# Optimization experiments

Hardware: AMD Instinct MI355X
Metric: run time of the kernel (lower is better)

The kernel has to match this reference:

```python
import jax, jax.numpy as jnp
import numpy as np

N_USERS = 100000
N_ITEMS = 50000
N_NODES = N_USERS + N_ITEMS
N_EDGES = 2400000
EMB = 64
LEAKY_ALPHA = 0.3  # tf.keras.layers.LeakyReLU default


def setup_inputs() -> dict:
    key = jax.random.key(0)
    ks = jax.random.split(key, 7)
    return {
        "user_emb": jax.random.normal(ks[0], (N_USERS, EMB), dtype=jnp.float32) * 0.1,
        "item_emb": jax.random.normal(ks[1], (N_ITEMS, EMB), dtype=jnp.float32) * 0.1,
        "W0": jax.random.normal(ks[2], (EMB, EMB), dtype=jnp.float32) * (1.0 / np.sqrt(EMB)),
        "W1": jax.random.normal(ks[3], (EMB, EMB), dtype=jnp.float32) * (1.0 / np.sqrt(EMB)),
        "adj_vals": jax.random.uniform(ks[4], (N_EDGES,), dtype=jnp.float32),
        "adj_rows": jax.random.randint(ks[5], (N_EDGES,), 0, N_NODES, dtype=jnp.int32),
        "adj_cols": jax.random.randint(ks[6], (N_EDGES,), 0, N_NODES, dtype=jnp.int32),
    }


def reference(user_emb, item_emb, W0, W1, adj_vals, adj_rows, adj_cols):
    n_users = user_emb.shape[0]
    n_nodes = n_users + item_emb.shape[0]

    def spmm(e):  # sparse adjacency @ dense embeddings, COO form
        # gather source-node features, scale by edge weight, scatter-add to dest rows
        return jax.ops.segment_sum(adj_vals[:, None] * e[adj_cols], adj_rows,
                                   num_segments=n_nodes)

    e0 = jnp.concatenate([user_emb, item_emb], axis=0)          # [N, d]
    # gcn[0] = GraphConv(W0): transpose(W0 @ (A@e)^T) == (A@e) @ W0^T
    e1 = spmm(e0) @ W0.T
    # gcn[1] = LeakyReLU (Keras default alpha=0.3)
    e2 = jnp.where(e1 >= 0, e1, LEAKY_ALPHA * e1)
    # gcn[2] = GraphConv(W1)
    e3 = spmm(e2) @ W1.T
    # stack+mean over the 4 embedding stages
    all_emb = (e0 + e1 + e2 + e3) * 0.25
    return all_emb[:n_users], all_emb[n_users:]
```

## Files before the change

kernel.cpp:

```cpp
#include <hip/hip_runtime.h>

#define N_USERS 100000
#define N_ITEMS 50000
#define N_NODES 150000
#define N_EDGES 2400000
#define EMB 64
#define LEAKY 0.3f

#define RB_SHIFT 8
#define RB (1 << RB_SHIFT)
#define NBKT ((N_NODES + RB - 1) >> RB_SHIFT)
#define L1_CHUNK 16384
#define NCH ((N_EDGES + L1_CHUNK - 1) / L1_CHUNK)
#define COL_MASK 0x3FFFFu
#define NTILE (N_NODES / 16)

typedef unsigned short u16;
typedef unsigned int   u32;
typedef __attribute__((ext_vector_type(8))) short short8v;
typedef __attribute__((ext_vector_type(4))) float f32x4;
typedef __attribute__((ext_vector_type(2))) float v2f;

__device__ __forceinline__ u16 f32_to_bf16_rne(float f) {
    u32 u = __float_as_uint(f);
    u32 r = (u + 0x7FFFu + ((u >> 16) & 1u)) >> 16;
    return (u16)r;
}
__device__ __forceinline__ float bf16_lo(u32 x) { return __uint_as_float(x << 16); }
__device__ __forceinline__ u32 pack_bf16(float lo, float hi) {
    return (u32)f32_to_bf16_rne(lo) | ((u32)f32_to_bf16_rne(hi) << 16);
}
__device__ __forceinline__ v2f up2(u32 w) {
    v2f r;
    r.x = __uint_as_float(w << 16);
    r.y = __uint_as_float(w & 0xFFFF0000u);
    return r;
}

__global__ __launch_bounds__(256) void conv_all(
    const float* __restrict__ uemb, const float* __restrict__ iemb,
    const float* __restrict__ W0, const float* __restrict__ W1,
    u16* __restrict__ ebf, u16* __restrict__ Wbf0, u16* __restrict__ Wbf1)
{
    const int gid = blockIdx.x * 256 + threadIdx.x;
    const int i = gid * 4;
    if (i < N_NODES * EMB) {
        const float* src = (i < N_USERS * EMB) ? uemb + i : iemb + (i - N_USERS * EMB);
        const float4 v = *(const float4*)src;
        ushort4 w;
        w.x = f32_to_bf16_rne(v.x);
        w.y = f32_to_bf16_rne(v.y);
        w.z = f32_to_bf16_rne(v.z);
        w.w = f32_to_bf16_rne(v.w);
        *(ushort4*)(ebf + i) = w;
    }
    if (gid < EMB * EMB) {
        Wbf0[gid] = f32_to_bf16_rne(W0[gid]);
        Wbf1[gid] = f32_to_bf16_rne(W1[gid]);
    }
}

__global__ __launch_bounds__(1024) void bkt_hist(
    const int* __restrict__ rows, int* __restrict__ H)
{
    __shared__ int cnt[NBKT];
    const int t = threadIdx.x;
    const int c = blockIdx.x;
    if (t < NBKT) cnt[t] = 0;
    __syncthreads();

    const int e0 = c * L1_CHUNK;
    const int e1 = (e0 + L1_CHUNK < N_EDGES) ? e0 + L1_CHUNK : N_EDGES;
    for (int i = e0 + t; i < e1; i += 1024)
        atomicAdd(&cnt[rows[i] >> RB_SHIFT], 1);
    __syncthreads();

    if (t < NBKT) H[c * NBKT + t] = cnt[t];
}

__global__ __launch_bounds__(1024) void scan_bkt(
    const int* __restrict__ H, int* __restrict__ bkt_ptr)
{
    __shared__ int lds[1024];
    const int t = threadIdx.x;

    int tot = 0;
    if (t < NBKT) {
        int a0 = 0, a1 = 0, a2 = 0, a3 = 0;
        int c = 0;
        for (; c + 4 <= NCH; c += 4) {
            a0 += H[(c + 0) * NBKT + t];
            a1 += H[(c + 1) * NBKT + t];
            a2 += H[(c + 2) * NBKT + t];
            a3 += H[(c + 3) * NBKT + t];
        }
        for (; c < NCH; ++c) a0 += H[c * NBKT + t];
        tot = (a0 + a1) + (a2 + a3);
    }
    lds[t] = (t < NBKT) ? tot : 0;
    __syncthreads();
    for (int off = 1; off < 1024; off <<= 1) {
        int x = 0;
        if (t >= off) x = lds[t - off];
        __syncthreads();
        lds[t] += x;
        __syncthreads();
    }
    if (t < NBKT) bkt_ptr[t] = lds[t] - tot;
    if (t == 0) bkt_ptr[NBKT] = N_EDGES;
}

__global__ __launch_bounds__(256) void fill_B(
    const int* __restrict__ H, const int* __restrict__ bkt_ptr,
    int* __restrict__ B)
{
    const int b = blockIdx.x * 256 + threadIdx.x;
    if (b >= NBKT) return;
    int run = bkt_ptr[b];
    int c = 0;
    for (; c + 4 <= NCH; c += 4) {
        const int h0 = H[(c + 0) * NBKT + b];
        const int h1 = H[(c + 1) * NBKT + b];
        const int h2 = H[(c + 2) * NBKT + b];
        const int h3 = H[(c + 3) * NBKT + b];
        B[(c + 0) * NBKT + b] = run;
        B[(c + 1) * NBKT + b] = run + h0;
        B[(c + 2) * NBKT + b] = run + h0 + h1;
        B[(c + 3) * NBKT + b] = run + h0 + h1 + h2;
        run += h0 + h1 + h2 + h3;
    }
    for (; c < NCH; ++c) {
        B[c * NBKT + b] = run;
        run += H[c * NBKT + b];
    }
}

__global__ __launch_bounds__(1024) void partition_l1(
    const float* __restrict__ vals, const int* __restrict__ rows,
    const int* __restrict__ cols, const int* __restrict__ B,
    float2* __restrict__ svc)
{
    __shared__ int base[NBKT];
    __shared__ int cnt[NBKT];
    const int t = threadIdx.x;
    const int c = blockIdx.x;
    if (t < NBKT) {
        base[t] = B[c * NBKT + t];
        cnt[t]  = 0;
    }
    __syncthreads();

    const int e0 = c * L1_CHUNK;
    const int e1 = (e0 + L1_CHUNK < N_EDGES) ? e0 + L1_CHUNK : N_EDGES;
    for (int i = e0 + t; i < e1; i += 1024) {
        const int r = rows[i];
        const int b = r >> RB_SHIFT;
        const int pos = base[b] + atomicAdd(&cnt[b], 1);
        const u32 packed = ((u32)(r & (RB - 1)) << 18) | (u32)cols[i];
        svc[pos] = make_float2(vals[i], __uint_as_float(packed));
    }
}

__global__ __launch_bounds__(512) void place_l2(
    const int* __restrict__ bkt_ptr, const float2* __restrict__ svc,
    float2* __restrict__ sedge, int* __restrict__ row_ptr)
{
    __shared__ int cnt[RB];
    __shared__ int heads[RB];
    const int b     = blockIdx.x;
    const int rbase = b << RB_SHIFT;
    const int t     = threadIdx.x;

    if (t < RB) cnt[t] = 0;
    __syncthreads();

    const int lo = bkt_ptr[b];
    const int hi = bkt_ptr[b + 1];

    for (int i = lo + t; i < hi; i += 512)
        atomicAdd(&cnt[__float_as_uint(svc[i].y) >> 18], 1);
    __syncthreads();

    int v = 0;
    if (t < RB) v = cnt[t];
    for (int off = 1; off < RB; off <<= 1) {
        int x = 0;
        if (t < RB && t >= off) x = cnt[t - off];
        __syncthreads();
        if (t < RB) cnt[t] += x;
        __syncthreads();
    }
    if (t < RB) {
        const int excl = cnt[t] - v;
        heads[t] = lo + excl;
        const int gr = rbase + t;
        if (gr <= N_NODES) row_ptr[gr] = lo + excl;
    }
    __syncthreads();

    for (int i = lo + t; i < hi; i += 512) {
        const float2 vc = svc[i];
        const int lr  = (int)(__float_as_uint(vc.y) >> 18);
        const int pos = atomicAdd(&heads[lr], 1);
        sedge[pos] = vc;
    }
}

__global__ __launch_bounds__(256) void spmm_bf16(
    const int* __restrict__ row_ptr,
    const float2* __restrict__ sedge,
    const u16* __restrict__ ebf,
    u16* __restrict__ tbf)
{
    const int tid  = threadIdx.x;
    const int lane = tid & 63;
    const int row  = blockIdx.x * 4 + (tid >> 6);
    if (row >= N_NODES) return;

    const int g = lane >> 3;
    const int q = lane & 7;

    const int beg = row_ptr[row];
    const int end = row_ptr[row + 1];

    v2f A0 = {0.f, 0.f}, A1 = {0.f, 0.f}, A2 = {0.f, 0.f}, A3 = {0.f, 0.f};

    for (int k = beg; k < end; k += 16) {
        const int  kA  = k + g;
        const int  kB  = k + 8 + g;
        const bool onA = kA < end;
        const bool onB = kB < end;
        const float2 mA = sedge[onA ? kA : end - 1];
        const float2 mB = sedge[onB ? kB : end - 1];
        const float vA = onA ? mA.x : 0.f;
        const float vB = onB ? mB.x : 0.f;
        const u32 iA = __float_as_uint(mA.y) & COL_MASK;
        const u32 iB = __float_as_uint(mB.y) & COL_MASK;
        const uint4 xA = *((const uint4*)(ebf + (size_t)iA * EMB) + q);
        const uint4 xB = *((const uint4*)(ebf + (size_t)iB * EMB) + q);
        const v2f vvA = {vA, vA};
        const v2f vvB = {vB, vB};
        A0 = vvA * up2(xA.x) + A0;
        A1 = vvA * up2(xA.y) + A1;
        A2 = vvA * up2(xA.z) + A2;
        A3 = vvA * up2(xA.w) + A3;
        A0 = vvB * up2(xB.x) + A0;
        A1 = vvB * up2(xB.y) + A1;
        A2 = vvB * up2(xB.z) + A2;
        A3 = vvB * up2(xB.w) + A3;
    }

    float s0 = A0.x, s1 = A0.y, s2 = A1.x, s3 = A1.y;
    float s4 = A2.x, s5 = A2.y, s6 = A3.x, s7 = A3.y;
    s0 += __shfl_xor(s0, 8); s0 += __shfl_xor(s0, 16); s0 += __shfl_xor(s0, 32);
    s1 += __shfl_xor(s1, 8); s1 += __shfl_xor(s1, 16); s1 += __shfl_xor(s1, 32);
    s2 += __shfl_xor(s2, 8); s2 += __shfl_xor(s2, 16); s2 += __shfl_xor(s2, 32);
    s3 += __shfl_xor(s3, 8); s3 += __shfl_xor(s3, 16); s3 += __shfl_xor(s3, 32);
    s4 += __shfl_xor(s4, 8); s4 += __shfl_xor(s4, 16); s4 += __shfl_xor(s4, 32);
    s5 += __shfl_xor(s5, 8); s5 += __shfl_xor(s5, 16); s5 += __shfl_xor(s5, 32);
    s6 += __shfl_xor(s6, 8); s6 += __shfl_xor(s6, 16); s6 += __shfl_xor(s6, 32);
    s7 += __shfl_xor(s7, 8); s7 += __shfl_xor(s7, 16); s7 += __shfl_xor(s7, 32);

    if (g == 0) {
        uint4 w;
        w.x = pack_bf16(s0, s1);
        w.y = pack_bf16(s2, s3);
        w.z = pack_bf16(s4, s5);
        w.w = pack_bf16(s6, s7);
        *(uint4*)(tbf + (size_t)row * EMB + 8 * q) = w;
    }
}

template <bool FIRST>
__global__ __launch_bounds__(256) void dense_mfma(
    const u16* __restrict__ tbf,
    const u16* __restrict__ Wbf,
    u16* ebf,
    u16* __restrict__ obf,
    float* __restrict__ out)
{
    const int tid  = threadIdx.x;
    const int l    = tid & 63;
    const int tile = blockIdx.x * 4 + (tid >> 6);
    if (tile >= NTILE) return;
    const int row0 = tile * 16;

    const int lr = l & 15;
    const int lk = l >> 4;

    short8v bfrag[4][2];
    #pragma unroll
    for (int c = 0; c < 4; ++c)
        #pragma unroll
        for (int kh = 0; kh < 2; ++kh)
            bfrag[c][kh] = *(const short8v*)(Wbf + (size_t)(16 * c + lr) * EMB
                                             + 32 * kh + 8 * lk);

    const u16* trow = tbf + (size_t)(row0 + lr) * EMB;
    const short8v afrag0 = *(const short8v*)(trow + 8 * lk);
    const short8v afrag1 = *(const short8v*)(trow + 32 + 8 * lk);

    f32x4 acc[4];
    #pragma unroll
    for (int c = 0; c < 4; ++c) {
        f32x4 z = {0.f, 0.f, 0.f, 0.f};
        z = __builtin_amdgcn_mfma_f32_16x16x32_bf16(afrag0, bfrag[c][0], z, 0, 0, 0);
        z = __builtin_amdgcn_mfma_f32_16x16x32_bf16(afrag1, bfrag[c][1], z, 0, 0, 0);
        acc[c] = z;
    }

    #pragma unroll
    for (int c = 0; c < 4; ++c) {
        #pragma unroll
        for (int r = 0; r < 4; ++r) {
            const int row = row0 + 4 * lk + r;
            const size_t idx = (size_t)row * EMB + 16 * c + lr;
            const float e1v = acc[c][r];
            if (FIRST) {
                const float e2v = (e1v >= 0.f) ? e1v : LEAKY * e1v;
                const float e0v = bf16_lo((u32)ebf[idx]);
                obf[idx] = f32_to_bf16_rne(0.25f * (e0v + e1v + e2v));
                ebf[idx] = f32_to_bf16_rne(e2v);
            } else {
                out[idx] = bf16_lo((u32)obf[idx]) + 0.25f * e1v;
            }
        }
    }
}

__global__ __launch_bounds__(256) void spmm_atomic(
    const float* __restrict__ vals, const int* __restrict__ rows,
    const int* __restrict__ cols, const float* __restrict__ src_a,
    const float* __restrict__ src_b, float* __restrict__ dst)
{
    const int tid  = threadIdx.x;
    const int lane = tid & 63;
    const int e    = blockIdx.x * 4 + (tid >> 6);
    if (e >= N_EDGES) return;
    const float v = vals[e];
    const int   c = cols[e];
    const int   r = rows[e];
    const float* src = (src_b != nullptr && c >= N_USERS)
                           ? src_b + (size_t)(c - N_USERS) * EMB
                           : src_a + (size_t)c * EMB;
    unsafeAtomicAdd(&dst[(size_t)r * EMB + lane], v * src[lane]);
}

template <bool FIRST>
__global__ __launch_bounds__(256) void dense_f32(
    const float* __restrict__ t, const float* __restrict__ W,
    const float* __restrict__ user_emb, const float* __restrict__ item_emb,
    float* __restrict__ e2, float* __restrict__ out)
{
    __shared__ float wT[64][65];
    __shared__ float trow[16][64];

    const int tid = threadIdx.x;
    for (int k = tid; k < 64 * 64; k += 256) {
        const int i = k >> 6, j = k & 63;
        wT[j][i] = W[k];
    }
    const int row_base = blockIdx.x * 16;
    for (int k = tid; k < 16 * 64; k += 256) {
        const int r = k >> 6, j = k & 63;
        const int row = row_base + r;
        trow[r][j] = (row < N_NODES) ? t[(size_t)row * EMB + j] : 0.f;
    }
    __syncthreads();

    const int i  = tid & 63;
    const int r0 = tid >> 6;

    #pragma unroll
    for (int rr = 0; rr < 4; ++rr) {
        const int r   = r0 * 4 + rr;
        const int row = row_base + r;
        if (row >= N_NODES) continue;
        float acc = 0.f;
        #pragma unroll
        for (int j = 0; j < 64; ++j)
            acc = fmaf(trow[r][j], wT[j][i], acc);
        const size_t idx = (size_t)row * EMB + i;
        if (FIRST) {
            const float e1v = acc;
            const float e2v = (e1v >= 0.f) ? e1v : LEAKY * e1v;
            const float e0v = (row < N_USERS)
                                  ? user_emb[idx]
                                  : item_emb[(size_t)(row - N_USERS) * EMB + i];
            e2[idx]  = e2v;
            out[idx] = 0.25f * (e0v + e1v + e2v);
        } else {
            out[idx] += 0.25f * acc;
        }
    }
}

extern "C" void kernel_launch(void* const* d_in, const int* in_sizes, int n_in,
                              void* d_out, int out_size, void* d_ws, size_t ws_size,
                              hipStream_t stream)
{
    const float* user_emb = (const float*)d_in[0];
    const float* item_emb = (const float*)d_in[1];
    const float* W0       = (const float*)d_in[2];
    const float* W1       = (const float*)d_in[3];
    const float* adj_vals = (const float*)d_in[4];
    const int*   adj_rows = (const int*)d_in[5];
    const int*   adj_cols = (const int*)d_in[6];
    float*       out      = (float*)d_out;

    const size_t mat_bytes = (size_t)N_NODES * EMB * sizeof(float);
    const size_t ebf_bytes = (size_t)N_NODES * EMB * sizeof(u16);
    const size_t edge8     = (size_t)N_EDGES * sizeof(float2);
    const size_t hmat      = (size_t)NCH * NBKT * sizeof(int);

    const size_t off_tbf    = 0;
    const size_t off_svc    = 0;
    const size_t off_sedge  = off_tbf + ebf_bytes;
    const size_t off_ebf    = off_sedge + edge8;
    const size_t off_obf    = off_ebf + ebf_bytes;
    const size_t off_rowptr = off_obf + ebf_bytes;
    const size_t off_H      = off_rowptr + (size_t)(N_NODES + 1) * sizeof(int);
    const size_t off_B      = off_H + hmat;
    const size_t off_ptr    = off_B + hmat;
    const size_t off_wbf    = (off_ptr + (size_t)(NBKT + 1) * sizeof(int) + 15) & ~(size_t)15;
    const size_t required   = off_wbf + 2 * (size_t)EMB * EMB * sizeof(u16);

    const int spmm_blocks   = (N_NODES + 3) / 4;
    const int densem_blocks = (NTILE + 3) / 4;
    const int conv_blocks   = (N_NODES * EMB / 4 + 255) / 256;

    if (ws_size >= required) {
        u16*    tbf     = (u16*)((char*)d_ws + off_tbf);
        float2* svc     = (float2*)((char*)d_ws + off_svc);
        float2* sedge   = (float2*)((char*)d_ws + off_sedge);
        u16*    ebf     = (u16*)((char*)d_ws + off_ebf);
        u16*    obf     = (u16*)((char*)d_ws + off_obf);
        int*    row_ptr = (int*)((char*)d_ws + off_rowptr);
        int*    H       = (int*)((char*)d_ws + off_H);
        int*    B       = (int*)((char*)d_ws + off_B);
        int*    bkt_ptr = (int*)((char*)d_ws + off_ptr);
        u16*    Wbf0    = (u16*)((char*)d_ws + off_wbf);
        u16*    Wbf1    = Wbf0 + EMB * EMB;

        conv_all<<<conv_blocks, 256, 0, stream>>>(
            user_emb, item_emb, W0, W1, ebf, Wbf0, Wbf1);

        bkt_hist<<<NCH, 1024, 0, stream>>>(adj_rows, H);
        scan_bkt<<<1, 1024, 0, stream>>>(H, bkt_ptr);
        fill_B<<<(NBKT + 255) / 256, 256, 0, stream>>>(H, bkt_ptr, B);
        partition_l1<<<NCH, 1024, 0, stream>>>(
            adj_vals, adj_rows, adj_cols, B, svc);
        place_l2<<<NBKT, 512, 0, stream>>>(bkt_ptr, svc, sedge, row_ptr);

        spmm_bf16<<<spmm_blocks, 256, 0, stream>>>(row_ptr, sedge, ebf, tbf);
        dense_mfma<true><<<densem_blocks, 256, 0, stream>>>(
            tbf, Wbf0, ebf, obf, out);

        spmm_bf16<<<spmm_blocks, 256, 0, stream>>>(row_ptr, sedge, ebf, tbf);
        dense_mfma<false><<<densem_blocks, 256, 0, stream>>>(
            tbf, Wbf1, ebf, obf, out);
    } else {
        float* t  = (float*)d_ws;
        float* e2 = (float*)((char*)d_ws + mat_bytes);
        const int dense_blocks = (N_NODES + 15) / 16;

        hipMemsetAsync(t, 0, mat_bytes, stream);
        spmm_atomic<<<(N_EDGES + 3) / 4, 256, 0, stream>>>(
            adj_vals, adj_rows, adj_cols, user_emb, item_emb, t);
        dense_f32<true><<<dense_blocks, 256, 0, stream>>>(
            t, W0, user_emb, item_emb, e2, out);

        hipMemsetAsync(t, 0, mat_bytes, stream);
        spmm_atomic<<<(N_EDGES + 3) / 4, 256, 0, stream>>>(
            adj_vals, adj_rows, adj_cols, e2, nullptr, t);
        dense_f32<false><<<dense_blocks, 256, 0, stream>>>(
            t, W1, nullptr, nullptr, nullptr, out);
    }
}
```

Measured before the change: 222.2 us.

## Fuse conversion with bucket histogram, merge scan with fill, stage placement in LDS

Result: faster. 209.2 us (-5.9%).

```diff
diff --git a/kernel.cpp b/kernel.cpp
--- a/kernel.cpp
+++ b/kernel.cpp
@@ -14,6 +14,7 @@
 #define NCH ((N_EDGES + L1_CHUNK - 1) / L1_CHUNK)
 #define COL_MASK 0x3FFFFu
 #define NTILE (N_NODES / 16)
+#define PCAP 6144
 
 typedef unsigned short u16;
 typedef unsigned int   u32;
@@ -37,49 +38,50 @@
     return r;
 }
 
-__global__ __launch_bounds__(256) void conv_all(
+__global__ __launch_bounds__(1024) void conv_hist(
     const float* __restrict__ uemb, const float* __restrict__ iemb,
     const float* __restrict__ W0, const float* __restrict__ W1,
-    u16* __restrict__ ebf, u16* __restrict__ Wbf0, u16* __restrict__ Wbf1)
-{
-    const int gid = blockIdx.x * 256 + threadIdx.x;
-    const int i = gid * 4;
-    if (i < N_NODES * EMB) {
-        const float* src = (i < N_USERS * EMB) ? uemb + i : iemb + (i - N_USERS * EMB);
-        const float4 v = *(const float4*)src;
-        ushort4 w;
-        w.x = f32_to_bf16_rne(v.x);
-        w.y = f32_to_bf16_rne(v.y);
-        w.z = f32_to_bf16_rne(v.z);
-        w.w = f32_to_bf16_rne(v.w);
-        *(ushort4*)(ebf + i) = w;
-    }
-    if (gid < EMB * EMB) {
-        Wbf0[gid] = f32_to_bf16_rne(W0[gid]);
-        Wbf1[gid] = f32_to_bf16_rne(W1[gid]);
-    }
-}
-
-__global__ __launch_bounds__(1024) void bkt_hist(
-    const int* __restrict__ rows, int* __restrict__ H)
+    const int* __restrict__ rows,
+    u16* __restrict__ ebf, u16* __restrict__ Wbf0, u16* __restrict__ Wbf1,
+    int* __restrict__ H)
 {
     __shared__ int cnt[NBKT];
     const int t = threadIdx.x;
-    const int c = blockIdx.x;
-    if (t < NBKT) cnt[t] = 0;
-    __syncthreads();
-
-    const int e0 = c * L1_CHUNK;
-    const int e1 = (e0 + L1_CHUNK < N_EDGES) ? e0 + L1_CHUNK : N_EDGES;
-    for (int i = e0 + t; i < e1; i += 1024)
-        atomicAdd(&cnt[rows[i] >> RB_SHIFT], 1);
-    __syncthreads();
-
-    if (t < NBKT) H[c * NBKT + t] = cnt[t];
-}
-
-__global__ __launch_bounds__(1024) void scan_bkt(
-    const int* __restrict__ H, int* __restrict__ bkt_ptr)
+    const int b = blockIdx.x;
+
+    if (b < NCH) {
+        if (t < NBKT) cnt[t] = 0;
+        __syncthreads();
+        const int e0 = b * L1_CHUNK;
+        const int e1 = (e0 + L1_CHUNK < N_EDGES) ? e0 + L1_CHUNK : N_EDGES;
+        for (int i = e0 + t; i < e1; i += 1024)
+            atomicAdd(&cnt[rows[i] >> RB_SHIFT], 1);
+        __syncthreads();
+        if (t < NBKT) H[b * NBKT + t] = cnt[t];
+    } else {
+        const int gid = (b - NCH) * 1024 + t;
+        const int i = gid * 4;
+        if (i < N_NODES * EMB) {
+            const float* src = (i < N_USERS * EMB) ? uemb + i
+                                                   : iemb + (i - N_USERS * EMB);
+            const float4 v = *(const float4*)src;
+            ushort4 w;
+            w.x = f32_to_bf16_rne(v.x);
+            w.y = f32_to_bf16_rne(v.y);
+            w.z = f32_to_bf16_rne(v.z);
+            w.w = f32_to_bf16_rne(v.w);
+            *(ushort4*)(ebf + i) = w;
+        }
+        if (gid < EMB * EMB) {
+            Wbf0[gid] = f32_to_bf16_rne(W0[gid]);
+            Wbf1[gid] = f32_to_bf16_rne(W1[gid]);
+        }
+    }
+}
+
+__global__ __launch_bounds__(1024) void scan_fill(
+    const int* __restrict__ H, int* __restrict__ bkt_ptr,
+    int* __restrict__ B)
 {
     __shared__ int lds[1024];
     const int t = threadIdx.x;
@@ -106,33 +108,29 @@
         lds[t] += x;
         __syncthreads();
     }
-    if (t < NBKT) bkt_ptr[t] = lds[t] - tot;
+    const int excl = lds[t] - tot;
+
+    if (t < NBKT) {
+        bkt_ptr[t] = excl;
+        int run = excl;
+        int c = 0;
+        for (; c + 4 <= NCH; c += 4) {
+            const int h0 = H[(c + 0) * NBKT + t];
+            const int h1 = H[(c + 1) * NBKT + t];
+            const int h2 = H[(c + 2) * NBKT + t];
+            const int h3 = H[(c + 3) * NBKT + t];
+            B[(c + 0) * NBKT + t] = run;
+            B[(c + 1) * NBKT + t] = run + h0;
+            B[(c + 2) * NBKT + t] = run + h0 + h1;
+            B[(c + 3) * NBKT + t] = run + h0 + h1 + h2;
+            run += h0 + h1 + h2 + h3;
+        }
+        for (; c < NCH; ++c) {
+            B[c * NBKT + t] = run;
+            run += H[c * NBKT + t];
+        }
+    }
     if (t == 0) bkt_ptr[NBKT] = N_EDGES;
-}
-
-__global__ __launch_bounds__(256) void fill_B(
-    const int* __restrict__ H, const int* __restrict__ bkt_ptr,
-    int* __restrict__ B)
-{
-    const int b = blockIdx.x * 256 + threadIdx.x;
-    if (b >= NBKT) return;
-    int run = bkt_ptr[b];
-    int c = 0;
-    for (; c + 4 <= NCH; c += 4) {
-        const int h0 = H[(c + 0) * NBKT + b];
-        const int h1 = H[(c + 1) * NBKT + b];
-        const int h2 = H[(c + 2) * NBKT + b];
-        const int h3 = H[(c + 3) * NBKT + b];
-        B[(c + 0) * NBKT + b] = run;
-        B[(c + 1) * NBKT + b] = run + h0;
-        B[(c + 2) * NBKT + b] = run + h0 + h1;
-        B[(c + 3) * NBKT + b] = run + h0 + h1 + h2;
-        run += h0 + h1 + h2 + h3;
-    }
-    for (; c < NCH; ++c) {
-        B[c * NBKT + b] = run;
-        run += H[c * NBKT + b];
-    }
 }
 
 __global__ __launch_bounds__(1024) void partition_l1(
@@ -165,6 +163,7 @@
     const int* __restrict__ bkt_ptr, const float2* __restrict__ svc,
     float2* __restrict__ sedge, int* __restrict__ row_ptr)
 {
+    __shared__ float2 E2[PCAP];
     __shared__ int cnt[RB];
     __shared__ int heads[RB];
     const int b     = blockIdx.x;
@@ -176,6 +175,7 @@
 
     const int lo = bkt_ptr[b];
     const int hi = bkt_ptr[b + 1];
+    const int n  = hi - lo;
 
     for (int i = lo + t; i < hi; i += 512)
         atomicAdd(&cnt[__float_as_uint(svc[i].y) >> 18], 1);
@@ -192,17 +192,29 @@
     }
     if (t < RB) {
         const int excl = cnt[t] - v;
-        heads[t] = lo + excl;
+        heads[t] = excl;
         const int gr = rbase + t;
         if (gr <= N_NODES) row_ptr[gr] = lo + excl;
     }
     __syncthreads();
 
-    for (int i = lo + t; i < hi; i += 512) {
-        const float2 vc = svc[i];
-        const int lr  = (int)(__float_as_uint(vc.y) >> 18);
-        const int pos = atomicAdd(&heads[lr], 1);
-        sedge[pos] = vc;
+    if (n <= PCAP) {
+        for (int i = lo + t; i < hi; i += 512) {
+            const float2 vc = svc[i];
+            const int lr  = (int)(__float_as_uint(vc.y) >> 18);
+            const int pos = atomicAdd(&heads[lr], 1);
+            E2[pos] = vc;
+        }
+        __syncthreads();
+        for (int i = t; i < n; i += 512)
+            sedge[lo + i] = E2[i];
+    } else {
+        for (int i = lo + t; i < hi; i += 512) {
+            const float2 vc = svc[i];
+            const int lr  = (int)(__float_as_uint(vc.y) >> 18);
+            const int pos = atomicAdd(&heads[lr], 1);
+            sedge[lo + pos] = vc;
+        }
     }
 }
 
@@ -427,7 +439,7 @@
 
     const int spmm_blocks   = (N_NODES + 3) / 4;
     const int densem_blocks = (NTILE + 3) / 4;
-    const int conv_blocks   = (N_NODES * EMB / 4 + 255) / 256;
+    const int convh_blocks  = NCH + (N_NODES * EMB / 4 + 1023) / 1024;
 
     if (ws_size >= required) {
         u16*    tbf     = (u16*)((char*)d_ws + off_tbf);
@@ -442,12 +454,10 @@
         u16*    Wbf0    = (u16*)((char*)d_ws + off_wbf);
         u16*    Wbf1    = Wbf0 + EMB * EMB;
 
-        conv_all<<<conv_blocks, 256, 0, stream>>>(
-            user_emb, item_emb, W0, W1, ebf, Wbf0, Wbf1);
-
-        bkt_hist<<<NCH, 1024, 0, stream>>>(adj_rows, H);
-        scan_bkt<<<1, 1024, 0, stream>>>(H, bkt_ptr);
-        fill_B<<<(NBKT + 255) / 256, 256, 0, stream>>>(H, bkt_ptr, B);
+        conv_hist<<<convh_blocks, 1024, 0, stream>>>(
+            user_emb, item_emb, W0, W1, adj_rows, ebf, Wbf0, Wbf1, H);
+
+        scan_fill<<<1, 1024, 0, stream>>>(H, bkt_ptr, B);
         partition_l1<<<NCH, 1024, 0, stream>>>(
             adj_vals, adj_rows, adj_cols, B, svc);
         place_l2<<<NBKT, 512, 0, stream>>>(bkt_ptr, svc, sedge, row_ptr);
```
